# Optimization experiments

Hardware: AMD Instinct MI355X
Metric: run time of the kernel (lower is better)

The kernel has to match this reference:

```python
import jax, jax.numpy as jnp
import numpy as np
from jax import lax

B = 32          # batch
L = 12          # n_blocks
HD = 768        # hidden_d
NH = 12         # n_heads
DH = HD // NH   # d_head = 64
NP = 14         # n_patches per side
S = NP * NP + 1 # seq len = 197
IN_D = 32 * 25  # 800, conv channels * 5x5 patch
OUT = 1000
EPS = 1e-5


def setup_inputs() -> dict:
    key = jax.random.key(0)
    ks = jax.random.split(key, 10)
    r = lambda k, s: jax.random.normal(k, s, jnp.float32) * 0.02
    return {
        "images": jax.random.normal(ks[0], (B, 3, 280, 280), jnp.float32),
        "conv_w": r(ks[1], (32, 3, 5, 5)),
        "conv_b": jnp.zeros((32,), jnp.float32),
        "bn_g": jnp.ones((32,), jnp.float32),
        "bn_b": jnp.zeros((32,), jnp.float32),
        "bn_m": jnp.zeros((32,), jnp.float32),
        "bn_v": jnp.ones((32,), jnp.float32),
        "map_w": r(ks[2], (HD, IN_D)),
        "map_b": jnp.zeros((HD,), jnp.float32),
        "cls_tok": jax.random.uniform(ks[3], (1, HD), jnp.float32),
        "ln_g": jnp.ones((L, HD), jnp.float32),
        "ln_b": jnp.zeros((L, HD), jnp.float32),
        "wq": r(ks[4], (L, NH, DH, DH)), "bq": jnp.zeros((L, NH, DH), jnp.float32),
        "wk": r(ks[5], (L, NH, DH, DH)), "bk": jnp.zeros((L, NH, DH), jnp.float32),
        "wv": r(ks[6], (L, NH, DH, DH)), "bv": jnp.zeros((L, NH, DH), jnp.float32),
        "mlp_w": r(ks[7], (OUT, HD)),
        "mlp_b": jnp.zeros((OUT,), jnp.float32),
    }


def _pos_emb(s, d):
    # pe[i,j] = sin(i/10000^(j/d)) if j even else cos(i/10000^((j-1)/d))
    i = jnp.arange(s, dtype=jnp.float32)[:, None]
    j = jnp.arange(d)[None, :]
    jf = j.astype(jnp.float32)
    ang_even = i / (10000.0 ** (jf / d))
    ang_odd = i / (10000.0 ** ((jf - 1.0) / d))
    return jnp.where(j % 2 == 0, jnp.sin(ang_even), jnp.cos(ang_odd))


def reference(images, conv_w, conv_b, bn_g, bn_b, bn_m, bn_v, map_w, map_b,
              cls_tok, ln_g, ln_b, wq, bq, wk, bk, wv, bv, mlp_w, mlp_b):
    # patch-embed conv: (B,3,280,280) -> (B,32,70,70)
    x = lax.conv_general_dilated(images, conv_w, (4, 4), [(1, 1), (1, 1)],
                                 dimension_numbers=('NCHW', 'OIHW', 'NCHW'))
    x = x + conv_b[None, :, None, None]
    # BatchNorm (eval) + ReLU; Dropout is identity in eval
    x = (x - bn_m[None, :, None, None]) * (bn_g / jnp.sqrt(bn_v + EPS))[None, :, None, None] \
        + bn_b[None, :, None, None]
    x = jax.nn.relu(x)
    n = x.shape[0]
    # split into 5x5 patches: (n,32,70,70) -> (n,196,800)
    x = x.reshape(n, 32, NP, 5, NP, 5).transpose(0, 2, 4, 1, 3, 5).reshape(n, NP * NP, IN_D)
    tok = x @ map_w.T + map_b                                   # (n,196,768)
    tok = jnp.concatenate([jnp.broadcast_to(cls_tok[None], (n, 1, HD)), tok], axis=1)
    out = tok + _pos_emb(S, HD)[None]                           # (n,197,768)
    scale = 1.0 / jnp.sqrt(jnp.float32(DH))
    for l in range(L):
        # LayerNorm
        mu = out.mean(-1, keepdims=True)
        var = out.var(-1, keepdims=True)
        h = (out - mu) / jnp.sqrt(var + EPS) * ln_g[l] + ln_b[l]
        xh = h.reshape(n, S, NH, DH)
        q = jnp.einsum('nshd,hed->nshe', xh, wq[l]) + bq[l]
        k = jnp.einsum('nshd,hed->nshe', xh, wk[l]) + bk[l]
        v = jnp.einsum('nshd,hed->nshe', xh, wv[l]) + bv[l]
        attn = jax.nn.softmax(jnp.einsum('nshe,nthe->nhst', q, k) * scale, axis=-1)
        o = jnp.einsum('nhst,nthe->nshe', attn, v).reshape(n, S, HD)
        out = out + o  # residual; NOTE: source block has no MLP sublayer
    cls = out[:, 0]
    return jax.nn.softmax(cls @ mlp_w.T + mlp_b, axis=-1)
```

## Files before the change

kernel.cpp:

```cpp
#include <hip/hip_runtime.h>

#define BB 32
#define LLAYERS 12
#define HDIM 768
#define NHEAD 12
#define DHEAD 64
#define SEQ 197
#define IND 800
#define NOUT 1000
#define EPSF 1e-5f
#define NTOK (BB * SEQ)
#define NPATCH (BB * 196)
#define SCALE 0.125f

typedef __attribute__((ext_vector_type(4))) float f32x4;
typedef __attribute__((ext_vector_type(8))) short short8;

static __device__ __forceinline__ ushort f2bf(float f) {
    union { float f; unsigned u; } v; v.f = f;
    unsigned r = v.u + 0x7FFFu + ((v.u >> 16) & 1u);
    return (ushort)(r >> 16);
}

static __device__ __forceinline__ void gload_lds16(const void* g, void* l) {
    __builtin_amdgcn_global_load_lds(
        (const __attribute__((address_space(1))) void*)g,
        (__attribute__((address_space(3))) void*)l, 16, 0, 0);
}

__global__ __launch_bounds__(256) void k_prep(
    const float* __restrict__ map_w, ushort* __restrict__ Wbf,
    const float* __restrict__ wq, const float* __restrict__ wk,
    const float* __restrict__ wv, ushort* __restrict__ Wswz,
    float* __restrict__ pos, const float* __restrict__ cls_tok,
    float* __restrict__ tok)
{
    int b = blockIdx.x;
    if (b < 600) {
        int i = b * 256 + threadIdx.x;
        if (i < (HDIM * IND) / 4) {
            float4 v = *(const float4*)&map_w[i * 4];
            ushort4 u = {f2bf(v.x), f2bf(v.y), f2bf(v.z), f2bf(v.w)};
            *(ushort4*)&Wbf[i * 4] = u;
        }
    } else if (b < 1464) {
        int t = (b - 600) * 256 + threadIdx.x;
        int lane = t & 63;
        int rest = t >> 6;
        int ktnt = rest & 7;
        int mlh = rest >> 3;
        int h = mlh % 12, ml = mlh / 12;
        int l = ml % 12, m = ml / 12;
        int nt = ktnt & 3, kt = ktnt >> 2;
        int e = nt * 16 + (lane & 15);
        int d = kt * 32 + (lane >> 4) * 8;
        const float* src = ((m == 0) ? wq : (m == 1) ? wk : wv)
                           + (((long)l * 12 + h) * 64 + e) * 64 + d;
        float4 a = *(const float4*)src;
        float4 bb = *(const float4*)(src + 4);
        short8 u;
        u[0] = (short)f2bf(a.x); u[1] = (short)f2bf(a.y);
        u[2] = (short)f2bf(a.z); u[3] = (short)f2bf(a.w);
        u[4] = (short)f2bf(bb.x); u[5] = (short)f2bf(bb.y);
        u[6] = (short)f2bf(bb.z); u[7] = (short)f2bf(bb.w);
        *(short8*)&Wswz[(long)mlh * 4096 + ktnt * 512 + lane * 8] = u;
    } else if (b < 1661) {
        int s = b - 1464;
        for (int e = threadIdx.x; e < HDIM; e += 256) {
            float freq = expf((float)(e & ~1) * (-9.210340371976184f / 768.0f));
            float ang = (float)s * freq;
            pos[s * HDIM + e] = (e & 1) ? cosf(ang) : sinf(ang);
        }
    } else {
        int n = b - 1661;
        for (int e = threadIdx.x; e < HDIM; e += 256)
            tok[(long)n * SEQ * HDIM + e] = cls_tok[e] + ((e & 1) ? 1.0f : 0.0f);
    }
}

__global__ __launch_bounds__(320) void k_conv_patch(
    const float* __restrict__ img, const float* __restrict__ cw,
    const float* __restrict__ cb, const float* __restrict__ bg,
    const float* __restrict__ bbias, const float* __restrict__ bm,
    const float* __restrict__ bvv, ushort* __restrict__ X)
{
    __shared__ float tile[2][3][21][21];
    __shared__ float w[2400];
    __shared__ float scale[32], shift[32];
    int tid = threadIdx.x;

    for (int i = tid; i < 2400; i += 320) w[i] = cw[i];
    if (tid < 32) {
        float sc = bg[tid] * rsqrtf(bvv[tid] + EPSF);
        scale[tid] = sc;
        shift[tid] = (cb[tid] - bm[tid]) * sc + bbias[tid];
    }
    for (int i = tid; i < 2 * 3 * 441; i += 320) {
        int pp = i / 1323, j = i % 1323;
        int c = j / 441, r = (j / 21) % 21, cc = j % 21;
        int gp = blockIdx.x * 2 + pp;
        int n = gp / 196, p = gp % 196;
        int h0 = (p / 14) * 20 - 1, w0 = (p % 14) * 20 - 1;
        int gh = h0 + r, gw = w0 + cc;
        float v = 0.f;
        if (gh >= 0 && gh < 280 && gw >= 0 && gw < 280)
            v = img[((long)(n * 3 + c) * 280 + gh) * 280 + gw];
        tile[pp][c][r][cc] = v;
    }
    __syncthreads();

    int pp = tid / 160, u = tid % 160;
    int c = u / 5, ph = u % 5;
    float acc[5] = {0.f, 0.f, 0.f, 0.f, 0.f};
    const float* wp = &w[c * 75];
    #pragma unroll
    for (int ci = 0; ci < 3; ci++) {
        #pragma unroll
        for (int kh = 0; kh < 5; kh++) {
            const float* row = &tile[pp][ci][ph * 4 + kh][0];
            float rv[21];
            #pragma unroll
            for (int j = 0; j < 21; j++) rv[j] = row[j];
            #pragma unroll
            for (int kw = 0; kw < 5; kw++) {
                float wv = wp[ci * 25 + kh * 5 + kw];
                #pragma unroll
                for (int pw = 0; pw < 5; pw++)
                    acc[pw] += rv[pw * 4 + kw] * wv;
            }
        }
    }
    int gp = blockIdx.x * 2 + pp;
    long ob = (long)gp * 800 + c * 25 + ph * 5;
    #pragma unroll
    for (int pw = 0; pw < 5; pw++) {
        float val = acc[pw] * scale[c] + shift[c];
        X[ob + pw] = f2bf(fmaxf(val, 0.f));
    }
}

__global__ __launch_bounds__(256, 2) void k_embed(
    const ushort* __restrict__ Xg, const ushort* __restrict__ Wg,
    const float* __restrict__ bias, const float* __restrict__ pos,
    float* __restrict__ tok)
{
    __shared__ __align__(16) ushort As[128 * 32];
    __shared__ __align__(16) ushort Bs[64 * 32];
    int m0 = blockIdx.x * 128, e0 = blockIdx.y * 64;
    int tid = threadIdx.x, lane = tid & 63, wave = tid >> 6;
    int col = lane & 15, quad = lane >> 4;
    int wm = (wave & 1) * 64, wn = (wave >> 1) * 32;
    int lr = lane >> 2, lc = (lane & 3) * 8;
    f32x4 zero4 = {0.f, 0.f, 0.f, 0.f};
    f32x4 acc[4][2];
    #pragma unroll
    for (int mt = 0; mt < 4; mt++)
        #pragma unroll
        for (int nt = 0; nt < 2; nt++) acc[mt][nt] = zero4;

    for (int k0 = 0; k0 < 800; k0 += 32) {
        __syncthreads();
        #pragma unroll
        for (int i = 0; i < 2; i++) {
            int c = wave * 2 + i;
            gload_lds16(&Xg[(long)(m0 + c * 16 + lr) * 800 + k0 + lc], &As[c * 512]);
        }
        {
            int c = wave;
            gload_lds16(&Wg[(long)(e0 + c * 16 + lr) * 800 + k0 + lc], &Bs[c * 512]);
        }
        __syncthreads();
        short8 a[4], b[2];
        #pragma unroll
        for (int mt = 0; mt < 4; mt++)
            a[mt] = *(const short8*)&As[(wm + mt * 16 + col) * 32 + quad * 8];
        #pragma unroll
        for (int nt = 0; nt < 2; nt++)
            b[nt] = *(const short8*)&Bs[(wn + nt * 16 + col) * 32 + quad * 8];
        #pragma unroll
        for (int mt = 0; mt < 4; mt++)
            #pragma unroll
            for (int nt = 0; nt < 2; nt++)
                acc[mt][nt] = __builtin_amdgcn_mfma_f32_16x16x32_bf16(a[mt], b[nt], acc[mt][nt], 0, 0, 0);
    }
    #pragma unroll
    for (int mt = 0; mt < 4; mt++) {
        #pragma unroll
        for (int r = 0; r < 4; r++) {
            int m = m0 + wm + mt * 16 + quad * 4 + r;
            int n = m / 196, s = m - n * 196 + 1;
            long rowb = ((long)n * SEQ + s) * HDIM;
            #pragma unroll
            for (int nt = 0; nt < 2; nt++) {
                int e = e0 + wn + nt * 16 + col;
                tok[rowb + e] = acc[mt][nt][r] + bias[e] + pos[s * HDIM + e];
            }
        }
    }
}

__global__ __launch_bounds__(256) void k_lnstats0(
    const float* __restrict__ tok, float* __restrict__ stats_out)
{
    int tid = threadIdx.x, lane = tid & 63, wave = tid >> 6;
    int row = blockIdx.x * 4 + wave;
    const float* p = tok + (long)row * HDIM;
    float s = 0.f, sq = 0.f;
    #pragma unroll
    for (int k = 0; k < 3; k++) {
        float4 v = *(const float4*)&p[k * 256 + lane * 4];
        s += v.x + v.y + v.z + v.w;
        sq += v.x * v.x + v.y * v.y + v.z * v.z + v.w * v.w;
    }
    #pragma unroll
    for (int off = 1; off < 64; off <<= 1) {
        s += __shfl_xor(s, off);
        sq += __shfl_xor(sq, off);
    }
    float* sp = &stats_out[(long)row * 24];
    if (lane == 0) { sp[0] = s; sp[1] = sq; }
    if (lane >= 2 && lane < 24) sp[lane] = 0.f;
}

__global__ __launch_bounds__(512, 4) void k_layer(
    float* __restrict__ tok,
    const float* __restrict__ stats_in, float* __restrict__ stats_out,
    const float* __restrict__ lng, const float* __restrict__ lnb,
    const ushort* __restrict__ wqs, const float* __restrict__ bqp,
    const ushort* __restrict__ wks, const float* __restrict__ bkp,
    const ushort* __restrict__ wvs, const float* __restrict__ bvp)
{
    __shared__ __align__(16) ushort Ks[208 * 72];
    __shared__ __align__(16) ushort Vt[64 * 232];
    __shared__ __align__(16) ushort Ps[8][16 * 72];
    __shared__ float smu[208], srstd[208];
    __shared__ __align__(16) float bias[3][64];
    __shared__ float lngs[64], lnbs[64];

    int h = blockIdx.x, n = blockIdx.y;
    int tid = threadIdx.x, lane = tid & 63, wave = tid >> 6;
    int col = lane & 15, quad = lane >> 4;
    int kq = quad * 4;
    f32x4 zero4 = {0.f, 0.f, 0.f, 0.f};

    if (tid < 192) {
        int m = tid >> 6, e = tid & 63;
        bias[m][e] = ((m == 0) ? bqp : (m == 1) ? bkp : bvp)[h * 64 + e];
    } else if (tid < 256) {
        lngs[tid - 192] = lng[h * 64 + tid - 192];
    } else if (tid < 320) {
        lnbs[tid - 256] = lnb[h * 64 + tid - 256];
    }
    for (int r = tid; r < SEQ; r += 512) {
        const float* sp = &stats_in[((long)n * SEQ + r) * 24];
        float s = 0.f, sq = 0.f;
        #pragma unroll
        for (int j = 0; j < 6; j++) {
            float4 v = *(const float4*)&sp[j * 4];
            s += v.x + v.z;
            sq += v.y + v.w;
        }
        float mu = s / 768.f;
        smu[r] = mu;
        srstd[r] = rsqrtf(sq / 768.f - mu * mu + EPSF);
    }
    for (int i = tid; i < 64 * 24; i += 512) {
        int e = i / 24, t = 208 + i % 24;
        Vt[e * 232 + t] = 0;
    }
    __syncthreads();

    long tokb = (long)n * SEQ * HDIM + h * 64;
    short8 a[2][2];
    #pragma unroll
    for (int sl = 0; sl < 2; sl++) {
        int st = sl * 8 + wave;
        if (st >= 13) continue;
        int row = st * 16 + col; if (row > SEQ - 1) row = SEQ - 1;
        float mu = smu[row], rs = srstd[row];
        #pragma unroll
        for (int kt = 0; kt < 2; kt++) {
            const float* tp = &tok[tokb + (long)row * HDIM + kt * 32 + quad * 8];
            float4 v0 = *(const float4*)tp;
            float4 v1 = *(const float4*)(tp + 4);
            const float* g = &lngs[kt * 32 + quad * 8];
            const float* bb = &lnbs[kt * 32 + quad * 8];
            short8 u;
            u[0] = (short)f2bf((v0.x - mu) * rs * g[0] + bb[0]);
            u[1] = (short)f2bf((v0.y - mu) * rs * g[1] + bb[1]);
            u[2] = (short)f2bf((v0.z - mu) * rs * g[2] + bb[2]);
            u[3] = (short)f2bf((v0.w - mu) * rs * g[3] + bb[3]);
            u[4] = (short)f2bf((v1.x - mu) * rs * g[4] + bb[4]);
            u[5] = (short)f2bf((v1.y - mu) * rs * g[5] + bb[5]);
            u[6] = (short)f2bf((v1.z - mu) * rs * g[6] + bb[6]);
            u[7] = (short)f2bf((v1.w - mu) * rs * g[7] + bb[7]);
            a[sl][kt] = u;
        }
    }

    ushort* myP = &Ps[wave][0];
    short8 aq[2][2];
    f32x4 bQ[4], bK[4];
    #pragma unroll
    for (int et = 0; et < 4; et++) {
        bQ[et] = *(const f32x4*)&bias[0][et * 16 + quad * 4];
        bK[et] = *(const f32x4*)&bias[1][et * 16 + quad * 4];
    }
    float bV[4];
    #pragma unroll
    for (int nt = 0; nt < 4; nt++) bV[nt] = bias[2][nt * 16 + col];

    #pragma unroll
    for (int m = 0; m < 3; m++) {
        const ushort* wp = ((m == 0) ? wqs : (m == 1) ? wks : wvs) + (long)h * 4096;
        short8 b[8];
        #pragma unroll
        for (int f = 0; f < 8; f++)
            b[f] = *(const short8*)&wp[f * 512 + lane * 8];
        #pragma unroll
        for (int sl = 0; sl < 2; sl++) {
            int st = sl * 8 + wave;
            if (st >= 13) continue;
            int q0 = st * 16;
            if (m < 2) {
                f32x4 acc[4] = {zero4, zero4, zero4, zero4};
                #pragma unroll
                for (int kt = 0; kt < 2; kt++)
                    #pragma unroll
                    for (int et = 0; et < 4; et++)
                        acc[et] = __builtin_amdgcn_mfma_f32_16x16x32_bf16(b[kt * 4 + et], a[sl][kt], acc[et], 0, 0, 0);
                if (m == 0) {
                    #pragma unroll
                    for (int et = 0; et < 4; et++) {
                        f32x4 bb = bQ[et];
                        ushort4 u = {f2bf(acc[et][0] + bb[0]), f2bf(acc[et][1] + bb[1]),
                                     f2bf(acc[et][2] + bb[2]), f2bf(acc[et][3] + bb[3])};
                        *(ushort4*)&myP[col * 72 + et * 16 + quad * 4] = u;
                    }
                    #pragma unroll
                    for (int kt = 0; kt < 2; kt++)
                        aq[sl][kt] = *(const short8*)&myP[col * 72 + kt * 32 + quad * 8];
                } else {
                    #pragma unroll
                    for (int et = 0; et < 4; et++) {
                        f32x4 bb = bK[et];
                        ushort4 u = {f2bf(acc[et][0] + bb[0]), f2bf(acc[et][1] + bb[1]),
                                     f2bf(acc[et][2] + bb[2]), f2bf(acc[et][3] + bb[3])};
                        *(ushort4*)&Ks[(q0 + col) * 72 + et * 16 + quad * 4] = u;
                    }
                }
            } else {
                f32x4 acc[4] = {zero4, zero4, zero4, zero4};
                #pragma unroll
                for (int kt = 0; kt < 2; kt++)
                    #pragma unroll
                    for (int nt = 0; nt < 4; nt++)
                        acc[nt] = __builtin_amdgcn_mfma_f32_16x16x32_bf16(a[sl][kt], b[kt * 4 + nt], acc[nt], 0, 0, 0);
                #pragma unroll
                for (int nt = 0; nt < 4; nt++) {
                    float bb = bV[nt];
                    ushort4 u = {f2bf(acc[nt][0] + bb), f2bf(acc[nt][1] + bb),
                                 f2bf(acc[nt][2] + bb), f2bf(acc[nt][3] + bb)};
                    *(ushort4*)&Vt[(nt * 16 + col) * 232 + q0 + quad * 4] = u;
                }
            }
        }
    }
    __syncthreads();

    #pragma unroll
    for (int sl = 0; sl < 2; sl++) {
        int st = sl * 8 + wave;
        if (st >= 13) continue;
        int q0 = st * 16;

        f32x4 sc[13];
        #pragma unroll
        for (int tt = 0; tt < 13; tt++) sc[tt] = zero4;
        #pragma unroll
        for (int tt = 0; tt < 13; tt++) {
            #pragma unroll
            for (int dt = 0; dt < 2; dt++) {
                short8 bk = *(const short8*)&Ks[(tt * 16 + col) * 72 + dt * 32 + quad * 8];
                sc[tt] = __builtin_amdgcn_mfma_f32_16x16x32_bf16(bk, aq[sl][dt], sc[tt], 0, 0, 0);
            }
        }

        float mx = -1e30f;
        #pragma unroll
        for (int tt = 0; tt < 12; tt++)
            #pragma unroll
            for (int r = 0; r < 4; r++) mx = fmaxf(mx, sc[tt][r]);
        #pragma unroll
        for (int r = 0; r < 4; r++)
            if (kq + r < 5) mx = fmaxf(mx, sc[12][r]);
        mx = fmaxf(mx, __shfl_xor(mx, 16));
        mx = fmaxf(mx, __shfl_xor(mx, 32));
        float s = 0.f;
        #pragma unroll
        for (int tt = 0; tt < 12; tt++)
            #pragma unroll
            for (int r = 0; r < 4; r++) {
                float e = __expf((sc[tt][r] - mx) * SCALE);
                sc[tt][r] = e; s += e;
            }
        #pragma unroll
        for (int r = 0; r < 4; r++) {
            float e = (kq + r < 5) ? __expf((sc[12][r] - mx) * SCALE) : 0.f;
            sc[12][r] = e; s += e;
        }
        s += __shfl_xor(s, 16);
        s += __shfl_xor(s, 32);
        float rinv = 1.f / s;

        f32x4 oacc[4];
        #pragma unroll
        for (int nt = 0; nt < 4; nt++) oacc[nt] = zero4;
        #pragma unroll
        for (int kt = 0; kt < 7; kt++) {
            #pragma unroll
            for (int half = 0; half < 2; half++) {
                int tt = kt * 2 + half;
                ushort4 u = {0, 0, 0, 0};
                if (tt < 13)
                    u = (ushort4){f2bf(sc[tt][0]), f2bf(sc[tt][1]),
                                  f2bf(sc[tt][2]), f2bf(sc[tt][3])};
                *(ushort4*)&myP[col * 72 + half * 16 + kq] = u;
            }
            short8 pa = *(const short8*)&myP[col * 72 + quad * 8];
            #pragma unroll
            for (int nt = 0; nt < 4; nt++) {
                short8 vb = *(const short8*)&Vt[(nt * 16 + col) * 232 + kt * 32 + quad * 8];
                oacc[nt] = __builtin_amdgcn_mfma_f32_16x16x32_bf16(pa, vb, oacc[nt], 0, 0, 0);
            }
        }

        float rv[4];
        #pragma unroll
        for (int r = 0; r < 4; r++) rv[r] = __shfl(rinv, kq + r, 16);

        #pragma unroll
        for (int r = 0; r < 4; r++) {
            int row = q0 + quad * 4 + r;
            float ss = 0.f, sq = 0.f;
            if (row < SEQ) {
                #pragma unroll
                for (int nt = 0; nt < 4; nt++) {
                    long o = ((long)n * SEQ + row) * HDIM + h * 64 + nt * 16 + col;
                    float nv = tok[o] + oacc[nt][r] * rv[r];
                    tok[o] = nv;
                    ss += nv; sq += nv * nv;
                }
            }
            #pragma unroll
            for (int off = 1; off < 16; off <<= 1) {
                ss += __shfl_xor(ss, off);
                sq += __shfl_xor(sq, off);
            }
            if (row < SEQ && col == 0) {
                float* sp = &stats_out[((long)n * SEQ + row) * 24 + h * 2];
                sp[0] = ss; sp[1] = sq;
            }
        }
    }
}

__global__ __launch_bounds__(256) void k_logits(
    const float* __restrict__ tok, const float* __restrict__ W,
    const float* __restrict__ b, float* __restrict__ logits)
{
    int n = blockIdx.x, oc = blockIdx.y;
    int tid = threadIdx.x, lane = tid & 63, wave = tid >> 6;
    const float* cp = &tok[(long)n * SEQ * HDIM];
    float4 c0 = *(const float4*)&cp[lane * 4];
    float4 c1 = *(const float4*)&cp[256 + lane * 4];
    float4 c2 = *(const float4*)&cp[512 + lane * 4];
    int obeg = oc * 125, oend = obeg + 125;
    for (int o = obeg + wave; o < oend; o += 4) {
        const float* wr = &W[(long)o * HDIM];
        float4 w0 = *(const float4*)&wr[lane * 4];
        float4 w1 = *(const float4*)&wr[256 + lane * 4];
        float4 w2 = *(const float4*)&wr[512 + lane * 4];
        float s = c0.x * w0.x + c0.y * w0.y + c0.z * w0.z + c0.w * w0.w
                + c1.x * w1.x + c1.y * w1.y + c1.z * w1.z + c1.w * w1.w
                + c2.x * w2.x + c2.y * w2.y + c2.z * w2.z + c2.w * w2.w;
        #pragma unroll
        for (int off = 1; off < 64; off <<= 1) s += __shfl_xor(s, off);
        if (lane == 0) logits[n * NOUT + o] = s + b[o];
    }
}

__global__ __launch_bounds__(256) void k_smax(
    const float* __restrict__ logits, float* __restrict__ out)
{
    __shared__ float lg[NOUT];
    __shared__ float red[256];
    int n = blockIdx.x, tid = threadIdx.x;
    for (int o = tid; o < NOUT; o += 256) lg[o] = logits[n * NOUT + o];
    __syncthreads();
    float m = -1e30f;
    for (int o = tid; o < NOUT; o += 256) m = fmaxf(m, lg[o]);
    red[tid] = m; __syncthreads();
    for (int off = 128; off > 0; off >>= 1) {
        if (tid < off) red[tid] = fmaxf(red[tid], red[tid + off]);
        __syncthreads();
    }
    float mx = red[0];
    __syncthreads();
    float s = 0.f;
    for (int o = tid; o < NOUT; o += 256) {
        float e = __expf(lg[o] - mx);
        lg[o] = e; s += e;
    }
    red[tid] = s; __syncthreads();
    for (int off = 128; off > 0; off >>= 1) {
        if (tid < off) red[tid] += red[tid + off];
        __syncthreads();
    }
    float inv = 1.f / red[0];
    for (int o = tid; o < NOUT; o += 256) out[(long)n * NOUT + o] = lg[o] * inv;
}

extern "C" void kernel_launch(void* const* d_in, const int* in_sizes, int n_in,
                              void* d_out, int out_size, void* d_ws, size_t ws_size,
                              hipStream_t stream)
{
    const float* images  = (const float*)d_in[0];
    const float* conv_w  = (const float*)d_in[1];
    const float* conv_b  = (const float*)d_in[2];
    const float* bn_g    = (const float*)d_in[3];
    const float* bn_b    = (const float*)d_in[4];
    const float* bn_m    = (const float*)d_in[5];
    const float* bn_v    = (const float*)d_in[6];
    const float* map_w   = (const float*)d_in[7];
    const float* map_b   = (const float*)d_in[8];
    const float* cls_tok = (const float*)d_in[9];
    const float* ln_g    = (const float*)d_in[10];
    const float* ln_b    = (const float*)d_in[11];
    const float* wq      = (const float*)d_in[12];
    const float* bq      = (const float*)d_in[13];
    const float* wk      = (const float*)d_in[14];
    const float* bk      = (const float*)d_in[15];
    const float* wv      = (const float*)d_in[16];
    const float* bv      = (const float*)d_in[17];
    const float* mlp_w   = (const float*)d_in[18];
    const float* mlp_b   = (const float*)d_in[19];
    float* out = (float*)d_out;

    const long SZ_X   = (long)NPATCH * IND;
    const long SZ_W   = (long)HDIM * IND;
    const long SZ_WS  = (long)3 * 144 * 4096;
    const long SZ_POS = (long)SEQ * HDIM;
    const long SZ_TOK = (long)NTOK * HDIM;
    const long SZ_ST  = (long)NTOK * 24;

    ushort* Xbf   = (ushort*)d_ws;
    ushort* Wbf   = Xbf + SZ_X;
    ushort* Wswz  = Wbf + SZ_W;
    float*  pos   = (float*)(Wswz + SZ_WS);
    float*  tok   = pos + SZ_POS;
    float*  sta   = tok + SZ_TOK;
    float*  stb   = sta + SZ_ST;
    float* logits = (float*)Xbf;

    k_prep<<<1693, 256, 0, stream>>>(map_w, Wbf, wq, wk, wv, Wswz,
                                     pos, cls_tok, tok);
    k_conv_patch<<<NPATCH / 2, 320, 0, stream>>>(images, conv_w, conv_b, bn_g,
                                                 bn_b, bn_m, bn_v, Xbf);
    dim3 ge(49, 12);
    k_embed<<<ge, 256, 0, stream>>>(Xbf, Wbf, map_b, pos, tok);

    k_lnstats0<<<NTOK / 4, 256, 0, stream>>>(tok, sta);
    for (int l = 0; l < LLAYERS; l++) {
        float* srd = (l & 1) ? stb : sta;
        float* swr = (l & 1) ? sta : stb;
        dim3 gl(12, 32);
        k_layer<<<gl, 512, 0, stream>>>(tok, srd, swr,
            ln_g + (long)l * HDIM, ln_b + (long)l * HDIM,
            Wswz + (long)(0 * 144 + l * 12) * 4096, bq + (long)l * NHEAD * DHEAD,
            Wswz + (long)(1 * 144 + l * 12) * 4096, bk + (long)l * NHEAD * DHEAD,
            Wswz + (long)(2 * 144 + l * 12) * 4096, bv + (long)l * NHEAD * DHEAD);
    }
    dim3 glo(BB, 8);
    k_logits<<<glo, 256, 0, stream>>>(tok, mlp_w, mlp_b, logits);
    k_smax<<<BB, 256, 0, stream>>>(logits, out);
}
```

Before: 516.8 us.

## Store token residual in head-major layout for contiguous per-head access

Changes the residual token buffer from (batch, seq, hidden) to (batch, head, seq, dhead), so each per-head layer block reads and writes a contiguous 197x64 slab instead of strided 64-float rows. The patch-embed epilogue, CLS init, LN stats kernel and logits kernel are updated to index the new layout. This aims to improve memory locality in the per-layer kernel, but the LN stats and logits kernels now gather across head slabs with strided accesses.

```diff
diff --git a/kernel.cpp b/kernel.cpp
--- a/kernel.cpp
+++ b/kernel.cpp
@@ -12,6 +12,7 @@
 #define NTOK (BB * SEQ)
 #define NPATCH (BB * 196)
 #define SCALE 0.125f
+#define HSTRIDE (SEQ * DHEAD)
 
 typedef __attribute__((ext_vector_type(4))) float f32x4;
 typedef __attribute__((ext_vector_type(8))) short short8;
@@ -27,6 +28,7 @@
         (const __attribute__((address_space(1))) void*)g,
         (__attribute__((address_space(3))) void*)l, 16, 0, 0);
 }
+
 
 __global__ __launch_bounds__(256) void k_prep(
     const float* __restrict__ map_w, ushort* __restrict__ Wbf,
@@ -73,8 +75,11 @@
         }
     } else {
         int n = b - 1661;
-        for (int e = threadIdx.x; e < HDIM; e += 256)
-            tok[(long)n * SEQ * HDIM + e] = cls_tok[e] + ((e & 1) ? 1.0f : 0.0f);
+        for (int e = threadIdx.x; e < HDIM; e += 256) {
+            int h = e >> 6, d = e & 63;
+            tok[(long)(n * 12 + h) * HSTRIDE + d] =
+                cls_tok[e] + ((e & 1) ? 1.0f : 0.0f);
+        }
     }
 }
 
@@ -183,17 +188,19 @@
             for (int nt = 0; nt < 2; nt++)
                 acc[mt][nt] = __builtin_amdgcn_mfma_f32_16x16x32_bf16(a[mt], b[nt], acc[mt][nt], 0, 0, 0);
     }
+    int hh = blockIdx.y;
     #pragma unroll
     for (int mt = 0; mt < 4; mt++) {
         #pragma unroll
         for (int r = 0; r < 4; r++) {
             int m = m0 + wm + mt * 16 + quad * 4 + r;
             int n = m / 196, s = m - n * 196 + 1;
-            long rowb = ((long)n * SEQ + s) * HDIM;
+            long rowb = ((long)(n * 12 + hh) * SEQ + s) * DHEAD;
             #pragma unroll
             for (int nt = 0; nt < 2; nt++) {
-                int e = e0 + wn + nt * 16 + col;
-                tok[rowb + e] = acc[mt][nt][r] + bias[e] + pos[s * HDIM + e];
+                int d = wn + nt * 16 + col;
+                int e = e0 + d;
+                tok[rowb + d] = acc[mt][nt][r] + bias[e] + pos[s * HDIM + e];
             }
         }
     }
@@ -204,11 +211,14 @@
 {
     int tid = threadIdx.x, lane = tid & 63, wave = tid >> 6;
     int row = blockIdx.x * 4 + wave;
-    const float* p = tok + (long)row * HDIM;
+    int n = row / SEQ, sidx = row - n * SEQ;
     float s = 0.f, sq = 0.f;
     #pragma unroll
     for (int k = 0; k < 3; k++) {
-        float4 v = *(const float4*)&p[k * 256 + lane * 4];
+        int i = k * 256 + lane * 4;
+        int h = i >> 6, d = i & 63;
+        const float* p = &tok[((long)(n * 12 + h) * SEQ + sidx) * DHEAD + d];
+        float4 v = *(const float4*)p;
         s += v.x + v.y + v.z + v.w;
         sq += v.x * v.x + v.y * v.y + v.z * v.z + v.w * v.w;
     }
@@ -270,7 +280,7 @@
     }
     __syncthreads();
 
-    long tokb = (long)n * SEQ * HDIM + h * 64;
+    long tokb = (long)(n * 12 + h) * HSTRIDE;
     short8 a[2][2];
     #pragma unroll
     for (int sl = 0; sl < 2; sl++) {
@@ -280,7 +290,7 @@
         float mu = smu[row], rs = srstd[row];
         #pragma unroll
         for (int kt = 0; kt < 2; kt++) {
-            const float* tp = &tok[tokb + (long)row * HDIM + kt * 32 + quad * 8];
+            const float* tp = &tok[tokb + (long)row * DHEAD + kt * 32 + quad * 8];
             float4 v0 = *(const float4*)tp;
             float4 v1 = *(const float4*)(tp + 4);
             const float* g = &lngs[kt * 32 + quad * 8];
@@ -446,7 +456,7 @@
             if (row < SEQ) {
                 #pragma unroll
                 for (int nt = 0; nt < 4; nt++) {
-                    long o = ((long)n * SEQ + row) * HDIM + h * 64 + nt * 16 + col;
+                    long o = tokb + (long)row * DHEAD + nt * 16 + col;
                     float nv = tok[o] + oacc[nt][r] * rv[r];
                     tok[o] = nv;
                     ss += nv; sq += nv * nv;
@@ -471,19 +481,22 @@
 {
     int n = blockIdx.x, oc = blockIdx.y;
     int tid = threadIdx.x, lane = tid & 63, wave = tid >> 6;
-    const float* cp = &tok[(long)n * SEQ * HDIM];
-    float4 c0 = *(const float4*)&cp[lane * 4];
-    float4 c1 = *(const float4*)&cp[256 + lane * 4];
-    float4 c2 = *(const float4*)&cp[512 + lane * 4];
+    float4 c[3];
+    #pragma unroll
+    for (int k = 0; k < 3; k++) {
+        int i = k * 256 + lane * 4;
+        int hh = i >> 6, d = i & 63;
+        c[k] = *(const float4*)&tok[(long)(n * 12 + hh) * HSTRIDE + d];
+    }
     int obeg = oc * 125, oend = obeg + 125;
     for (int o = obeg + wave; o < oend; o += 4) {
         const float* wr = &W[(long)o * HDIM];
         float4 w0 = *(const float4*)&wr[lane * 4];
         float4 w1 = *(const float4*)&wr[256 + lane * 4];
         float4 w2 = *(const float4*)&wr[512 + lane * 4];
-        float s = c0.x * w0.x + c0.y * w0.y + c0.z * w0.z + c0.w * w0.w
-                + c1.x * w1.x + c1.y * w1.y + c1.z * w1.z + c1.w * w1.w
-                + c2.x * w2.x + c2.y * w2.y + c2.z * w2.z + c2.w * w2.w;
+        float s = c[0].x * w0.x + c[0].y * w0.y + c[0].z * w0.z + c[0].w * w0.w
+                + c[1].x * w1.x + c[1].y * w1.y + c[1].z * w1.z + c[1].w * w1.w
+                + c[2].x * w2.x + c[2].y * w2.y + c[2].z * w2.z + c[2].w * w2.w;
         #pragma unroll
         for (int off = 1; off < 64; off <<= 1) s += __shfl_xor(s, off);
         if (lane == 0) logits[n * NOUT + o] = s + b[o];
```

Result: no change. 514.0 us, median of 2 (-0.5%).
